# Kernel optimization log

Hardware: AMD Instinct MI355X
Metric: run time of the kernel (lower is better)

The kernel has to match this reference:

```python
import jax, jax.numpy as jnp
import numpy as np

B, S, D_IN = 4, 2048, 1024
EMBED, HEADS = 1024, 16
HEAD_DIM = EMBED // HEADS


def setup_inputs() -> dict:
    key = jax.random.key(0)
    k1, k2, k3 = jax.random.split(key, 3)
    x = jax.random.normal(k1, (B, S, D_IN), dtype=jnp.float32)
    # xavier-uniform-ish init scales
    lim_qkv = float(np.sqrt(6.0 / (D_IN + 3 * EMBED)))
    lim_o = float(np.sqrt(6.0 / (EMBED + EMBED)))
    w_qkv = jax.random.uniform(k2, (3 * EMBED, D_IN), minval=-lim_qkv, maxval=lim_qkv, dtype=jnp.float32)
    b_qkv = jnp.zeros((3 * EMBED,), dtype=jnp.float32)
    w_o = jax.random.uniform(k3, (EMBED, EMBED), minval=-lim_o, maxval=lim_o, dtype=jnp.float32)
    b_o = jnp.zeros((EMBED,), dtype=jnp.float32)
    return {"x": x, "w_qkv": w_qkv, "b_qkv": b_qkv, "w_o": w_o, "b_o": b_o}


def reference(x, w_qkv, b_qkv, w_o, b_o):
    b, s, _ = x.shape
    qkv = jnp.einsum('bsi,oi->bso', x, w_qkv) + b_qkv            # (b, s, 3E)
    qkv = qkv.reshape(b, s, HEADS, 3 * HEAD_DIM).transpose(0, 2, 1, 3)  # (b, h, s, 3d)
    q, k, v = jnp.split(qkv, 3, axis=-1)                          # each (b, h, s, d)
    scale = 1.0 / jnp.sqrt(jnp.float32(HEAD_DIM))
    attn = jnp.einsum('bhqd,bhkd->bhqk', q, k) * scale            # (b, h, s, s)
    attn = jax.nn.softmax(attn, axis=-1)
    vals = jnp.einsum('bhqk,bhkd->bhqd', attn, v)                 # (b, h, s, d)
    # NOTE: original torch code reshapes (b,h,s,d) -> (b,s,e) WITHOUT transposing
    # heads back; jnp.reshape reproduces that flattening exactly.
    vals = vals.reshape(b, s, EMBED)
    out = jnp.einsum('bse,oe->bso', vals, w_o) + b_o              # (b, s, E)
    return out
```

## Files before the change

### kernel.cpp

```cpp
#include <hip/hip_runtime.h>
#include <stdint.h>
#include <stddef.h>

#define DEVINL __device__ __forceinline__

typedef unsigned short u16;
typedef unsigned int u32;
typedef __attribute__((ext_vector_type(8))) short short8;
typedef __attribute__((ext_vector_type(4))) float f32x4;
typedef __attribute__((ext_vector_type(4))) u32 u32x4;
typedef __attribute__((ext_vector_type(2))) u32 u32x2;

#define QSCALE 0.18033688011112042f

DEVINL u16 f2bf(float f) {
    u32 u = __builtin_bit_cast(u32, f);
    u32 r = (u + 0x7fffu + ((u >> 16) & 1u)) >> 16;
    return (u16)r;
}

DEVINL void gld_lds16(const void* g, void* l) {
    __builtin_amdgcn_global_load_lds(
        (__attribute__((address_space(1))) u32*)(uintptr_t)g,
        (__attribute__((address_space(3))) u32*)l, 16, 0, 0);
}

DEVINL u32 pack_bf16_trunc(float lo, float hi) {
    return __builtin_amdgcn_perm(__builtin_bit_cast(u32, hi),
                                 __builtin_bit_cast(u32, lo), 0x07060302u);
}

DEVINL void plswap32(u32 &a, u32 &b) {
#if __has_builtin(__builtin_amdgcn_permlane32_swap)
    u32x2 r = __builtin_amdgcn_permlane32_swap(a, b, false, false);
    a = r[0]; b = r[1];
#else
    asm("v_permlane32_swap_b32 %0, %1" : "+v"(a), "+v"(b));
#endif
}
DEVINL void plswap16(u32 &a, u32 &b) {
#if __has_builtin(__builtin_amdgcn_permlane16_swap)
    u32x2 r = __builtin_amdgcn_permlane16_swap(a, b, false, false);
    a = r[0]; b = r[1];
#else
    asm("v_permlane16_swap_b32 %0, %1" : "+v"(a), "+v"(b));
#endif
}

__global__ void prep_inputs(const float* __restrict__ x, const float* __restrict__ wqkv,
                            const float* __restrict__ bqkv, const float* __restrict__ wo,
                            u16* __restrict__ xb, u16* __restrict__ wqb,
                            u16* __restrict__ wob, float* __restrict__ bsc) {
    int blk = blockIdx.x;
    if (blk < 6144) {
        const float* src; u16* dst; int base; bool qscale = false;
        if (blk < 4096)      { src = x;    dst = xb;  base = blk; }
        else if (blk < 5632) { src = wqkv; dst = wqb; base = blk - 4096; qscale = true; }
        else                 { src = wo;   dst = wob; base = blk - 5632; }
        int i = (base * 256 + threadIdx.x) * 8;
        float sc = 1.0f;
        if (qscale) { int row = i >> 10; if ((row % 192) < 64) sc = QSCALE; }
        float4 a = *(const float4*)(src + i);
        float4 c = *(const float4*)(src + i + 4);
        union { u16 s[8]; u32x4 v; } t;
        t.s[0] = f2bf(a.x * sc); t.s[1] = f2bf(a.y * sc); t.s[2] = f2bf(a.z * sc); t.s[3] = f2bf(a.w * sc);
        t.s[4] = f2bf(c.x * sc); t.s[5] = f2bf(c.y * sc); t.s[6] = f2bf(c.z * sc); t.s[7] = f2bf(c.w * sc);
        *(u32x4*)(dst + i) = t.v;
    } else {
        int i = (blk - 6144) * 256 + threadIdx.x;
        float sc = ((i % 192) < 64) ? QSCALE : 1.0f;
        bsc[i] = bqkv[i] * sc;
    }
}

__global__ void gemm_qkv(const u16* __restrict__ A, const u16* __restrict__ Bm,
                         const float* __restrict__ bias, u16* __restrict__ qkvb,
                         u16* __restrict__ vtb) {
    const int K = 1024, N = 3072;
    __shared__ u16 As[128 * 64];
    __shared__ u16 Bs[128 * 64];
    const int tid = threadIdx.x;
    const int lane = tid & 63;
    const int wv = tid >> 6, wr = wv >> 1, wc = wv & 1;
    const int l15 = lane & 15, quad = lane >> 4;
    const int e7 = (l15 & 7) * 8;
    const int id = blockIdx.x;
    const int xcd = id & 7, rr = id >> 3;
    const int m0 = ((xcd << 3) + rr / 24) * 128;
    const int n0 = (rr % 24) * 128;

    f32x4 acc[4][4];
#pragma unroll
    for (int i = 0; i < 4; i++)
#pragma unroll
        for (int j = 0; j < 4; j++) acc[i][j] = (f32x4){0.f, 0.f, 0.f, 0.f};

    const u16* Ab = A + (size_t)m0 * K;
    const u16* Bb = Bm + (size_t)n0 * K;
    const int lrow = lane >> 3;
    const int lgr  = (lane & 7) ^ lrow;
    const int r0   = wv * 8 + lrow;

    for (int k0 = 0; k0 < K; k0 += 64) {
#pragma unroll
        for (int j = 0; j < 4; j++) {
            int row = j * 32 + r0;
            gld_lds16(Ab + (size_t)row * K + k0 + lgr * 8, (char*)As + (size_t)(j * 256 + tid) * 16);
            gld_lds16(Bb + (size_t)row * K + k0 + lgr * 8, (char*)Bs + (size_t)(j * 256 + tid) * 16);
        }
        __syncthreads();
#pragma unroll
        for (int ks = 0; ks < 2; ks++) {
            short8 af[4], bf8[4];
#pragma unroll
            for (int mi = 0; mi < 4; mi++)
                af[mi] = *(const short8*)(As + (wr * 64 + mi * 16 + l15) * 64 + ((ks * 32 + quad * 8) ^ e7));
#pragma unroll
            for (int ni = 0; ni < 4; ni++)
                bf8[ni] = *(const short8*)(Bs + (wc * 64 + ni * 16 + l15) * 64 + ((ks * 32 + quad * 8) ^ e7));
#pragma unroll
            for (int mi = 0; mi < 4; mi++)
#pragma unroll
                for (int ni = 0; ni < 4; ni++)
                    acc[mi][ni] = __builtin_amdgcn_mfma_f32_16x16x32_bf16(af[mi], bf8[ni], acc[mi][ni], 0, 0, 0);
        }
        __syncthreads();
    }

#pragma unroll
    for (int mi = 0; mi < 4; mi++) {
        int row_b = m0 + wr * 64 + mi * 16 + quad * 4;
#pragma unroll
        for (int ni = 0; ni < 4; ni++) {
            int c0 = n0 + wc * 64 + ni * 16;
            int sec0 = c0 % 192;
            float bv = bias[c0 + l15];
            float v0 = acc[mi][ni][0] + bv;
            float v1 = acc[mi][ni][1] + bv;
            float v2 = acc[mi][ni][2] + bv;
            float v3 = acc[mi][ni][3] + bv;
            if (sec0 >= 128) {
                int hh = c0 / 192;
                int b = row_b >> 11;
                int s = row_b & 2047;
                int d = sec0 - 128 + l15;
                u32 lo = (u32)f2bf(v0) | ((u32)f2bf(v1) << 16);
                u32 hi = (u32)f2bf(v2) | ((u32)f2bf(v3) << 16);
                *(u32x2*)(vtb + ((size_t)((b * 16 + hh) * 64 + d)) * 2048 + s) = (u32x2){lo, hi};
            } else {
                int col = c0 + l15;
                qkvb[(size_t)(row_b + 0) * N + col] = f2bf(v0);
                qkvb[(size_t)(row_b + 1) * N + col] = f2bf(v1);
                qkvb[(size_t)(row_b + 2) * N + col] = f2bf(v2);
                qkvb[(size_t)(row_b + 3) * N + col] = f2bf(v3);
            }
        }
    }
}

__global__ void gemm_out(const u16* __restrict__ A, const u16* __restrict__ Bm,
                         const float* __restrict__ bias, float* __restrict__ C) {
    const int K = 1024, N = 1024;
    __shared__ u16 As[128 * 64];
    __shared__ u16 Bs[64 * 64];
    const int tid = threadIdx.x;
    const int lane = tid & 63;
    const int wv = tid >> 6, wr = wv >> 1, wc = wv & 1;
    const int l15 = lane & 15, quad = lane >> 4;
    const int e7 = (l15 & 7) * 8;
    const int id = blockIdx.x;
    const int xcd = id & 7, rr = id >> 3;
    const int m0 = ((xcd << 3) + (rr >> 4)) * 128;
    const int n0 = (rr & 15) * 64;

    f32x4 acc[4][2];
#pragma unroll
    for (int i = 0; i < 4; i++)
#pragma unroll
        for (int j = 0; j < 2; j++) acc[i][j] = (f32x4){0.f, 0.f, 0.f, 0.f};

    const u16* Ab = A + (size_t)m0 * K;
    const u16* Bb = Bm + (size_t)n0 * K;
    const int lrow = lane >> 3;
    const int lgr  = (lane & 7) ^ lrow;
    const int r0   = wv * 8 + lrow;

    for (int k0 = 0; k0 < K; k0 += 64) {
#pragma unroll
        for (int j = 0; j < 4; j++)
            gld_lds16(Ab + (size_t)(j * 32 + r0) * K + k0 + lgr * 8,
                      (char*)As + (size_t)(j * 256 + tid) * 16);
#pragma unroll
        for (int j = 0; j < 2; j++)
            gld_lds16(Bb + (size_t)(j * 32 + r0) * K + k0 + lgr * 8,
                      (char*)Bs + (size_t)(j * 256 + tid) * 16);
        __syncthreads();
#pragma unroll
        for (int ks = 0; ks < 2; ks++) {
            short8 af[4], bf8[2];
#pragma unroll
            for (int mi = 0; mi < 4; mi++)
                af[mi] = *(const short8*)(As + (wr * 64 + mi * 16 + l15) * 64 + ((ks * 32 + quad * 8) ^ e7));
#pragma unroll
            for (int ni = 0; ni < 2; ni++)
                bf8[ni] = *(const short8*)(Bs + (wc * 32 + ni * 16 + l15) * 64 + ((ks * 32 + quad * 8) ^ e7));
#pragma unroll
            for (int mi = 0; mi < 4; mi++)
#pragma unroll
                for (int ni = 0; ni < 2; ni++)
                    acc[mi][ni] = __builtin_amdgcn_mfma_f32_16x16x32_bf16(af[mi], bf8[ni], acc[mi][ni], 0, 0, 0);
        }
        __syncthreads();
    }

#pragma unroll
    for (int mi = 0; mi < 4; mi++) {
        int row_b = m0 + wr * 64 + mi * 16 + quad * 4;
#pragma unroll
        for (int ni = 0; ni < 2; ni++) {
            int col = n0 + wc * 32 + ni * 16 + l15;
            float bv = bias[col];
#pragma unroll
            for (int r = 0; r < 4; r++)
                C[(size_t)(row_b + r) * N + col] = acc[mi][ni][r] + bv;
        }
    }
}

__launch_bounds__(512, 4)
__global__ void flash_attn(const u16* __restrict__ qkv, const u16* __restrict__ vt,
                           u16* __restrict__ vals2) {
    __shared__ u16 Ks[2][64 * 64];
    __shared__ u16 Vts[2][64 * 64];

    const int tid = threadIdx.x;
    const int lane = tid & 63, wv = tid >> 6;
    const int l15 = lane & 15, quad = lane >> 4;
    const int e7 = (l15 & 7) * 8;
    const int id = blockIdx.x;
    const int m = id >> 3;
    const int bh = ((id & 7) << 3) + (m >> 3);
    const int s0 = (m & 7) << 8;
    const int b = bh >> 4, h = bh & 15;

    short8 qf[2][2];
    const u16* qbase = qkv + (size_t)(b * 2048 + s0 + wv * 32) * 3072 + h * 192;
#pragma unroll
    for (int qi = 0; qi < 2; qi++)
#pragma unroll
        for (int ks = 0; ks < 2; ks++)
            qf[qi][ks] = *(const short8*)(qbase + (size_t)(qi * 16 + l15) * 3072 + ks * 32 + quad * 8);

    f32x4 o_acc[2][4];
    f32x4 sum_acc[2];
#pragma unroll
    for (int qi = 0; qi < 2; qi++) {
        sum_acc[qi] = (f32x4){0.f, 0.f, 0.f, 0.f};
#pragma unroll
        for (int nd = 0; nd < 4; nd++) o_acc[qi][nd] = (f32x4){0.f, 0.f, 0.f, 0.f};
    }
    const f32x4 fzero = (f32x4){0.f, 0.f, 0.f, 0.f};

    const u16* kg = qkv + (size_t)(b * 2048) * 3072 + h * 192 + 64;
    const u16* vg = vt + (size_t)bh * 64 * 2048;

    const int lrow = lane >> 3;
    const int lgr  = (lane & 7) ^ lrow;
    const int r0   = wv * 8 + lrow;

    const short8 ones = (short8){0x3F80, 0x3F80, 0x3F80, 0x3F80, 0x3F80, 0x3F80, 0x3F80, 0x3F80};

    gld_lds16(kg + (size_t)r0 * 3072 + lgr * 8, (char*)&Ks[0][0] + (size_t)tid * 16);
    gld_lds16(vg + (size_t)r0 * 2048 + lgr * 8, (char*)&Vts[0][0] + (size_t)tid * 16);
    __syncthreads();

    int cur = 0;
    for (int kb = 0; kb < 2048; kb += 64) {
        if (kb + 64 < 2048) {
            int nb = cur ^ 1;
            gld_lds16(kg + (size_t)(kb + 64 + r0) * 3072 + lgr * 8,
                      (char*)&Ks[nb][0] + (size_t)tid * 16);
            gld_lds16(vg + (size_t)r0 * 2048 + kb + 64 + lgr * 8,
                      (char*)&Vts[nb][0] + (size_t)tid * 16);
        }

        f32x4 s_acc[4][2];
        __builtin_amdgcn_s_setprio(1);
#pragma unroll
        for (int ki = 0; ki < 4; ki++) {
            short8 kf0 = *(const short8*)(&Ks[cur][0] + (ki * 16 + l15) * 64 + ((quad * 8) ^ e7));
            short8 kf1 = *(const short8*)(&Ks[cur][0] + (ki * 16 + l15) * 64 + ((32 + quad * 8) ^ e7));
#pragma unroll
            for (int qi = 0; qi < 2; qi++)
                s_acc[ki][qi] = __builtin_amdgcn_mfma_f32_16x16x32_bf16(kf0, qf[qi][0], fzero, 0, 0, 0);
#pragma unroll
            for (int qi = 0; qi < 2; qi++)
                s_acc[ki][qi] = __builtin_amdgcn_mfma_f32_16x16x32_bf16(kf1, qf[qi][1], s_acc[ki][qi], 0, 0, 0);
        }
        __builtin_amdgcn_s_setprio(0);

        short8 ap[2][2];
#pragma unroll
        for (int c = 0; c < 2; c++)
#pragma unroll
            for (int qi = 0; qi < 2; qi++) {
                u32 w0 = pack_bf16_trunc(__builtin_amdgcn_exp2f(s_acc[2 * c][qi][0]),
                                         __builtin_amdgcn_exp2f(s_acc[2 * c][qi][1]));
                u32 w1 = pack_bf16_trunc(__builtin_amdgcn_exp2f(s_acc[2 * c][qi][2]),
                                         __builtin_amdgcn_exp2f(s_acc[2 * c][qi][3]));
                u32 w2 = pack_bf16_trunc(__builtin_amdgcn_exp2f(s_acc[2 * c + 1][qi][0]),
                                         __builtin_amdgcn_exp2f(s_acc[2 * c + 1][qi][1]));
                u32 w3 = pack_bf16_trunc(__builtin_amdgcn_exp2f(s_acc[2 * c + 1][qi][2]),
                                         __builtin_amdgcn_exp2f(s_acc[2 * c + 1][qi][3]));
                plswap32(w0, w2);
                plswap32(w1, w3);
                plswap16(w0, w2);
                plswap16(w1, w3);
                u32x4 wf = (u32x4){w0, w1, w2, w3};
                ap[qi][c] = __builtin_bit_cast(short8, wf);
            }

#pragma unroll
        for (int c = 0; c < 2; c++) {
#pragma unroll
            for (int qi = 0; qi < 2; qi++)
                sum_acc[qi] = __builtin_amdgcn_mfma_f32_16x16x32_bf16(ap[qi][c], ones, sum_acc[qi], 0, 0, 0);
            __builtin_amdgcn_s_setprio(1);
#pragma unroll
            for (int nd = 0; nd < 4; nd++) {
                short8 bv = *(const short8*)(&Vts[cur][0] + (nd * 16 + l15) * 64 + ((c * 32 + quad * 8) ^ e7));
#pragma unroll
                for (int qi = 0; qi < 2; qi++)
                    o_acc[qi][nd] = __builtin_amdgcn_mfma_f32_16x16x32_bf16(ap[qi][c], bv, o_acc[qi][nd], 0, 0, 0);
            }
            __builtin_amdgcn_s_setprio(0);
        }

        __syncthreads();
        cur ^= 1;
    }

#pragma unroll
    for (int qi = 0; qi < 2; qi++) {
        f32x4 inv;
#pragma unroll
        for (int r = 0; r < 4; r++) inv[r] = 1.0f / sum_acc[qi][r];
#pragma unroll
        for (int nd = 0; nd < 4; nd++) {
            int d = nd * 16 + l15;
#pragma unroll
            for (int r = 0; r < 4; r++) {
                int s = s0 + wv * 32 + qi * 16 + quad * 4 + r;
                size_t row2 = (size_t)(b * 2048 + h * 128 + (s >> 4));
                int col2 = ((s & 15) << 6) + d;
                vals2[row2 * 1024 + col2] = f2bf(o_acc[qi][nd][r] * inv[r]);
            }
        }
    }
}

extern "C" void kernel_launch(void* const* d_in, const int* in_sizes, int n_in,
                              void* d_out, int out_size, void* d_ws, size_t ws_size,
                              hipStream_t stream) {
    (void)in_sizes; (void)n_in; (void)out_size; (void)ws_size;
    const float* x      = (const float*)d_in[0];
    const float* w_qkv  = (const float*)d_in[1];
    const float* b_qkv  = (const float*)d_in[2];
    const float* w_o    = (const float*)d_in[3];
    const float* b_o    = (const float*)d_in[4];
    float* out = (float*)d_out;

    char* ws = (char*)d_ws;
    u16* xb   = (u16*)(ws);
    u16* wqb  = (u16*)(ws + 16777216);
    u16* wob  = (u16*)(ws + 23068672);
    u16* qkvb = (u16*)(ws + 25165824);
    u16* vtb  = (u16*)(ws + 75497472);
    u16* v2b  = (u16*)(ws + 92274688);
    float* bsc = (float*)(ws + 92274688);

    prep_inputs<<<6156, 256, 0, stream>>>(x, w_qkv, b_qkv, w_o, xb, wqb, wob, bsc);

    gemm_qkv<<<1536, 256, 0, stream>>>(xb, wqb, bsc, qkvb, vtb);

    flash_attn<<<512, 512, 0, stream>>>(qkvb, vtb, v2b);

    gemm_out<<<1024, 256, 0, stream>>>(v2b, wob, b_o, out);
}
```

Measured before the change: 242.4 us.

## Widen output GEMM tile to 128x128 and process 128 keys per attention stage

The output projection GEMM moves from 128x64 to 128x128 tiles with 4x4 MFMA accumulators per wave, halving the grid and improving operand reuse per LDS load. The flash attention kernel now loads two 64-key sub-tiles per pipeline stage, doubling LDS buffers, so it issues half as many barriers and prefetch rounds. The cost is more LDS per block and more accumulator registers, which may lower occupancy. The 512-block GEMM grid may also underfill the device.

```diff
diff --git a/kernel.cpp b/kernel.cpp
--- a/kernel.cpp
+++ b/kernel.cpp
@@ -162,7 +162,7 @@
                          const float* __restrict__ bias, float* __restrict__ C) {
     const int K = 1024, N = 1024;
     __shared__ u16 As[128 * 64];
-    __shared__ u16 Bs[64 * 64];
+    __shared__ u16 Bs[128 * 64];
     const int tid = threadIdx.x;
     const int lane = tid & 63;
     const int wv = tid >> 6, wr = wv >> 1, wc = wv & 1;
@@ -170,14 +170,14 @@
     const int e7 = (l15 & 7) * 8;
     const int id = blockIdx.x;
     const int xcd = id & 7, rr = id >> 3;
-    const int m0 = ((xcd << 3) + (rr >> 4)) * 128;
-    const int n0 = (rr & 15) * 64;
-
-    f32x4 acc[4][2];
+    const int m0 = ((xcd << 3) + (rr >> 3)) * 128;
+    const int n0 = (rr & 7) * 128;
+
+    f32x4 acc[4][4];
 #pragma unroll
     for (int i = 0; i < 4; i++)
 #pragma unroll
-        for (int j = 0; j < 2; j++) acc[i][j] = (f32x4){0.f, 0.f, 0.f, 0.f};
+        for (int j = 0; j < 4; j++) acc[i][j] = (f32x4){0.f, 0.f, 0.f, 0.f};
 
     const u16* Ab = A + (size_t)m0 * K;
     const u16* Bb = Bm + (size_t)n0 * K;
@@ -187,27 +187,25 @@
 
     for (int k0 = 0; k0 < K; k0 += 64) {
 #pragma unroll
-        for (int j = 0; j < 4; j++)
-            gld_lds16(Ab + (size_t)(j * 32 + r0) * K + k0 + lgr * 8,
-                      (char*)As + (size_t)(j * 256 + tid) * 16);
-#pragma unroll
-        for (int j = 0; j < 2; j++)
-            gld_lds16(Bb + (size_t)(j * 32 + r0) * K + k0 + lgr * 8,
-                      (char*)Bs + (size_t)(j * 256 + tid) * 16);
+        for (int j = 0; j < 4; j++) {
+            int row = j * 32 + r0;
+            gld_lds16(Ab + (size_t)row * K + k0 + lgr * 8, (char*)As + (size_t)(j * 256 + tid) * 16);
+            gld_lds16(Bb + (size_t)row * K + k0 + lgr * 8, (char*)Bs + (size_t)(j * 256 + tid) * 16);
+        }
         __syncthreads();
 #pragma unroll
         for (int ks = 0; ks < 2; ks++) {
-            short8 af[4], bf8[2];
+            short8 af[4], bf8[4];
 #pragma unroll
             for (int mi = 0; mi < 4; mi++)
                 af[mi] = *(const short8*)(As + (wr * 64 + mi * 16 + l15) * 64 + ((ks * 32 + quad * 8) ^ e7));
 #pragma unroll
-            for (int ni = 0; ni < 2; ni++)
-                bf8[ni] = *(const short8*)(Bs + (wc * 32 + ni * 16 + l15) * 64 + ((ks * 32 + quad * 8) ^ e7));
+            for (int ni = 0; ni < 4; ni++)
+                bf8[ni] = *(const short8*)(Bs + (wc * 64 + ni * 16 + l15) * 64 + ((ks * 32 + quad * 8) ^ e7));
 #pragma unroll
             for (int mi = 0; mi < 4; mi++)
 #pragma unroll
-                for (int ni = 0; ni < 2; ni++)
+                for (int ni = 0; ni < 4; ni++)
                     acc[mi][ni] = __builtin_amdgcn_mfma_f32_16x16x32_bf16(af[mi], bf8[ni], acc[mi][ni], 0, 0, 0);
         }
         __syncthreads();
@@ -217,8 +215,8 @@
     for (int mi = 0; mi < 4; mi++) {
         int row_b = m0 + wr * 64 + mi * 16 + quad * 4;
 #pragma unroll
-        for (int ni = 0; ni < 2; ni++) {
-            int col = n0 + wc * 32 + ni * 16 + l15;
+        for (int ni = 0; ni < 4; ni++) {
+            int col = n0 + wc * 64 + ni * 16 + l15;
             float bv = bias[col];
 #pragma unroll
             for (int r = 0; r < 4; r++)
@@ -230,8 +228,8 @@
 __launch_bounds__(512, 4)
 __global__ void flash_attn(const u16* __restrict__ qkv, const u16* __restrict__ vt,
                            u16* __restrict__ vals2) {
-    __shared__ u16 Ks[2][64 * 64];
-    __shared__ u16 Vts[2][64 * 64];
+    __shared__ u16 Ks[2][2][64 * 64];
+    __shared__ u16 Vts[2][2][64 * 64];
 
     const int tid = threadIdx.x;
     const int lane = tid & 63, wv = tid >> 6;
@@ -270,70 +268,84 @@
 
     const short8 ones = (short8){0x3F80, 0x3F80, 0x3F80, 0x3F80, 0x3F80, 0x3F80, 0x3F80, 0x3F80};
 
-    gld_lds16(kg + (size_t)r0 * 3072 + lgr * 8, (char*)&Ks[0][0] + (size_t)tid * 16);
-    gld_lds16(vg + (size_t)r0 * 2048 + lgr * 8, (char*)&Vts[0][0] + (size_t)tid * 16);
+#pragma unroll
+    for (int st = 0; st < 2; st++) {
+        gld_lds16(kg + (size_t)(st * 64 + r0) * 3072 + lgr * 8,
+                  (char*)&Ks[0][st][0] + (size_t)tid * 16);
+        gld_lds16(vg + (size_t)r0 * 2048 + st * 64 + lgr * 8,
+                  (char*)&Vts[0][st][0] + (size_t)tid * 16);
+    }
     __syncthreads();
 
     int cur = 0;
-    for (int kb = 0; kb < 2048; kb += 64) {
-        if (kb + 64 < 2048) {
+    for (int kb = 0; kb < 2048; kb += 128) {
+        if (kb + 128 < 2048) {
             int nb = cur ^ 1;
-            gld_lds16(kg + (size_t)(kb + 64 + r0) * 3072 + lgr * 8,
-                      (char*)&Ks[nb][0] + (size_t)tid * 16);
-            gld_lds16(vg + (size_t)r0 * 2048 + kb + 64 + lgr * 8,
-                      (char*)&Vts[nb][0] + (size_t)tid * 16);
-        }
-
-        f32x4 s_acc[4][2];
-        __builtin_amdgcn_s_setprio(1);
-#pragma unroll
-        for (int ki = 0; ki < 4; ki++) {
-            short8 kf0 = *(const short8*)(&Ks[cur][0] + (ki * 16 + l15) * 64 + ((quad * 8) ^ e7));
-            short8 kf1 = *(const short8*)(&Ks[cur][0] + (ki * 16 + l15) * 64 + ((32 + quad * 8) ^ e7));
-#pragma unroll
-            for (int qi = 0; qi < 2; qi++)
-                s_acc[ki][qi] = __builtin_amdgcn_mfma_f32_16x16x32_bf16(kf0, qf[qi][0], fzero, 0, 0, 0);
-#pragma unroll
-            for (int qi = 0; qi < 2; qi++)
-                s_acc[ki][qi] = __builtin_amdgcn_mfma_f32_16x16x32_bf16(kf1, qf[qi][1], s_acc[ki][qi], 0, 0, 0);
-        }
-        __builtin_amdgcn_s_setprio(0);
-
-        short8 ap[2][2];
-#pragma unroll
-        for (int c = 0; c < 2; c++)
-#pragma unroll
-            for (int qi = 0; qi < 2; qi++) {
-                u32 w0 = pack_bf16_trunc(__builtin_amdgcn_exp2f(s_acc[2 * c][qi][0]),
-                                         __builtin_amdgcn_exp2f(s_acc[2 * c][qi][1]));
-                u32 w1 = pack_bf16_trunc(__builtin_amdgcn_exp2f(s_acc[2 * c][qi][2]),
-                                         __builtin_amdgcn_exp2f(s_acc[2 * c][qi][3]));
-                u32 w2 = pack_bf16_trunc(__builtin_amdgcn_exp2f(s_acc[2 * c + 1][qi][0]),
-                                         __builtin_amdgcn_exp2f(s_acc[2 * c + 1][qi][1]));
-                u32 w3 = pack_bf16_trunc(__builtin_amdgcn_exp2f(s_acc[2 * c + 1][qi][2]),
-                                         __builtin_amdgcn_exp2f(s_acc[2 * c + 1][qi][3]));
-                plswap32(w0, w2);
-                plswap32(w1, w3);
-                plswap16(w0, w2);
-                plswap16(w1, w3);
-                u32x4 wf = (u32x4){w0, w1, w2, w3};
-                ap[qi][c] = __builtin_bit_cast(short8, wf);
+#pragma unroll
+            for (int st = 0; st < 2; st++) {
+                gld_lds16(kg + (size_t)(kb + 128 + st * 64 + r0) * 3072 + lgr * 8,
+                          (char*)&Ks[nb][st][0] + (size_t)tid * 16);
+                gld_lds16(vg + (size_t)r0 * 2048 + kb + 128 + st * 64 + lgr * 8,
+                          (char*)&Vts[nb][st][0] + (size_t)tid * 16);
             }
-
-#pragma unroll
-        for (int c = 0; c < 2; c++) {
-#pragma unroll
-            for (int qi = 0; qi < 2; qi++)
-                sum_acc[qi] = __builtin_amdgcn_mfma_f32_16x16x32_bf16(ap[qi][c], ones, sum_acc[qi], 0, 0, 0);
+        }
+
+#pragma unroll
+        for (int st = 0; st < 2; st++) {
+            const u16* Kc = &Ks[cur][st][0];
+            const u16* Vc = &Vts[cur][st][0];
+
+            f32x4 s_acc[4][2];
             __builtin_amdgcn_s_setprio(1);
 #pragma unroll
-            for (int nd = 0; nd < 4; nd++) {
-                short8 bv = *(const short8*)(&Vts[cur][0] + (nd * 16 + l15) * 64 + ((c * 32 + quad * 8) ^ e7));
+            for (int ki = 0; ki < 4; ki++) {
+                short8 kf0 = *(const short8*)(Kc + (ki * 16 + l15) * 64 + ((quad * 8) ^ e7));
+                short8 kf1 = *(const short8*)(Kc + (ki * 16 + l15) * 64 + ((32 + quad * 8) ^ e7));
 #pragma unroll
                 for (int qi = 0; qi < 2; qi++)
-                    o_acc[qi][nd] = __builtin_amdgcn_mfma_f32_16x16x32_bf16(ap[qi][c], bv, o_acc[qi][nd], 0, 0, 0);
+                    s_acc[ki][qi] = __builtin_amdgcn_mfma_f32_16x16x32_bf16(kf0, qf[qi][0], fzero, 0, 0, 0);
+#pragma unroll
+                for (int qi = 0; qi < 2; qi++)
+                    s_acc[ki][qi] = __builtin_amdgcn_mfma_f32_16x16x32_bf16(kf1, qf[qi][1], s_acc[ki][qi], 0, 0, 0);
             }
             __builtin_amdgcn_s_setprio(0);
+
+            short8 ap[2][2];
+#pragma unroll
+            for (int c = 0; c < 2; c++)
+#pragma unroll
+                for (int qi = 0; qi < 2; qi++) {
+                    u32 w0 = pack_bf16_trunc(__builtin_amdgcn_exp2f(s_acc[2 * c][qi][0]),
+                                             __builtin_amdgcn_exp2f(s_acc[2 * c][qi][1]));
+                    u32 w1 = pack_bf16_trunc(__builtin_amdgcn_exp2f(s_acc[2 * c][qi][2]),
+                                             __builtin_amdgcn_exp2f(s_acc[2 * c][qi][3]));
+                    u32 w2 = pack_bf16_trunc(__builtin_amdgcn_exp2f(s_acc[2 * c + 1][qi][0]),
+                                             __builtin_amdgcn_exp2f(s_acc[2 * c + 1][qi][1]));
+                    u32 w3 = pack_bf16_trunc(__builtin_amdgcn_exp2f(s_acc[2 * c + 1][qi][2]),
+                                             __builtin_amdgcn_exp2f(s_acc[2 * c + 1][qi][3]));
+                    plswap32(w0, w2);
+                    plswap32(w1, w3);
+                    plswap16(w0, w2);
+                    plswap16(w1, w3);
+                    u32x4 wf = (u32x4){w0, w1, w2, w3};
+                    ap[qi][c] = __builtin_bit_cast(short8, wf);
+                }
+
+#pragma unroll
+            for (int c = 0; c < 2; c++) {
+#pragma unroll
+                for (int qi = 0; qi < 2; qi++)
+                    sum_acc[qi] = __builtin_amdgcn_mfma_f32_16x16x32_bf16(ap[qi][c], ones, sum_acc[qi], 0, 0, 0);
+                __builtin_amdgcn_s_setprio(1);
+#pragma unroll
+                for (int nd = 0; nd < 4; nd++) {
+                    short8 bv = *(const short8*)(Vc + (nd * 16 + l15) * 64 + ((c * 32 + quad * 8) ^ e7));
+#pragma unroll
+                    for (int qi = 0; qi < 2; qi++)
+                        o_acc[qi][nd] = __builtin_amdgcn_mfma_f32_16x16x32_bf16(ap[qi][c], bv, o_acc[qi][nd], 0, 0, 0);
+                }
+                __builtin_amdgcn_s_setprio(0);
+            }
         }
 
         __syncthreads();
@@ -385,5 +397,5 @@
 
     flash_attn<<<512, 512, 0, stream>>>(qkvb, vtb, v2b);
 
-    gemm_out<<<1024, 256, 0, stream>>>(v2b, wob, b_o, out);
-}
+    gemm_out<<<512, 256, 0, stream>>>(v2b, wob, b_o, out);
+}
```

Result: no change. 244.5 us (+0.8%).
